# Kernel optimization log

Hardware: AMD Instinct MI355X
Metric: run time of the kernel (lower is better)

Reference implementation:

```python
import jax, jax.numpy as jnp
import numpy as np

B, N, D = 8, 2048, 768
LN_EPS = 1e-5


def setup_inputs() -> dict:
    key = jax.random.key(0)
    ks = jax.random.split(key, 5)
    scale = 1.0 / np.sqrt(D)
    features = jax.random.normal(ks[0], (B, N, D), dtype=jnp.float32)
    mask = jax.random.randint(ks[1], (B, N), 0, 2) == 1  # True = masked (padding)
    Wq = jax.random.normal(ks[2], (D, D), dtype=jnp.float32) * scale
    Wk = jax.random.normal(ks[3], (D, D), dtype=jnp.float32) * scale
    Wv = jax.random.normal(ks[4], (D, D), dtype=jnp.float32) * scale
    ln_gamma = jnp.ones((D,), dtype=jnp.float32)
    ln_beta = jnp.zeros((D,), dtype=jnp.float32)
    return {"features": features, "mask": mask, "Wq": Wq, "Wk": Wk, "Wv": Wv,
            "ln_gamma": ln_gamma, "ln_beta": ln_beta}


def reference(features, mask, Wq, Wk, Wv, ln_gamma, ln_beta):
    # LayerNorm over last dim
    mu = jnp.mean(features, axis=-1, keepdims=True)
    var = jnp.mean(jnp.square(features - mu), axis=-1, keepdims=True)
    x = (features - mu) * jax.lax.rsqrt(var + LN_EPS) * ln_gamma + ln_beta
    # torch Linear: y = x @ W.T
    Q = jnp.einsum('bnd,ed->bne', x, Wq)
    K = jnp.einsum('bnd,ed->bne', x, Wk)
    V = jnp.einsum('bnd,ed->bne', x, Wv)
    scale = x.shape[-1] ** -0.5
    scores = jnp.einsum('bnd,bmd->bnm', Q, K) * scale  # [B,N,N]
    scores = jnp.where(mask[:, None, :], -jnp.inf, scores)
    probs = jax.nn.softmax(scores, axis=-1)
    ctx = jnp.einsum('bnm,bmd->bnd', probs, V)
    return ctx
```

## Files before the change

### kernel.cpp

```cpp
#include <hip/hip_runtime.h>
#include <hip/hip_bf16.h>
#include <cstdint>

typedef __attribute__((ext_vector_type(8))) __bf16 bf16v8;
typedef __attribute__((ext_vector_type(4))) float f32x4;
typedef __attribute__((ext_vector_type(4))) unsigned short ushort4v;
typedef __attribute__((ext_vector_type(8))) unsigned short ushort8v;

#define BB 8
#define NN 2048
#define DD 768

__device__ __forceinline__ float b2f(unsigned short u) {
  union { unsigned int i; float f; } c; c.i = ((unsigned int)u) << 16; return c.f;
}
__device__ __forceinline__ unsigned short f2b(float f) {
  union { float f; unsigned int i; } c; c.f = f;
  unsigned int u = c.i;
  return (unsigned short)((u + 0x7fffu + ((u >> 16) & 1u)) >> 16);
}

__global__ __launch_bounds__(256) void ln_kernel(const float* __restrict__ x,
                                                 const float* __restrict__ gamma,
                                                 const float* __restrict__ beta,
                                                 unsigned short* __restrict__ xb) {
  int row = blockIdx.x;
  const float* xr = x + (size_t)row * DD;
  int t = threadIdx.x;
  float a0 = xr[t], a1 = xr[t + 256], a2 = xr[t + 512];
  float s = a0 + a1 + a2;
  float q = a0 * a0 + a1 * a1 + a2 * a2;
  for (int o = 32; o > 0; o >>= 1) { s += __shfl_xor(s, o); q += __shfl_xor(q, o); }
  __shared__ float red[2][4];
  int w = t >> 6, lane = t & 63;
  if (lane == 0) { red[0][w] = s; red[1][w] = q; }
  __syncthreads();
  s = red[0][0] + red[0][1] + red[0][2] + red[0][3];
  q = red[1][0] + red[1][1] + red[1][2] + red[1][3];
  float mean = s * (1.0f / DD);
  float var = q * (1.0f / DD) - mean * mean;
  float inv = rsqrtf(var + 1e-5f);
  unsigned short* o0 = xb + (size_t)row * DD;
  o0[t]       = f2b((a0 - mean) * inv * gamma[t]       + beta[t]);
  o0[t + 256] = f2b((a1 - mean) * inv * gamma[t + 256] + beta[t + 256]);
  o0[t + 512] = f2b((a2 - mean) * inv * gamma[t + 512] + beta[t + 512]);
}

__global__ __launch_bounds__(256) void wconvert(const float* __restrict__ Wq,
                                                const float* __restrict__ Wk,
                                                const float* __restrict__ Wv,
                                                unsigned short* __restrict__ Wcat) {
  int i = blockIdx.x * 256 + threadIdx.x;
  const int dd = DD * DD;
  if (i >= 3 * dd) return;
  float v;
  if (i < dd)           v = Wq[i] * 0.03608439182435161f;
  else if (i < 2 * dd)  v = Wk[i - dd];
  else                  v = Wv[i - 2 * dd];
  Wcat[i] = f2b(v);
}

__global__ __launch_bounds__(256) void mask_scan(const int* __restrict__ mask,
                                                 int* __restrict__ kidx,
                                                 int* __restrict__ ncnt) {
  int b = blockIdx.x;
  const int* mr = mask + b * NN;
  int t = threadIdx.x;
#pragma unroll
  for (int j = 0; j < 8; ++j) kidx[b * NN + t * 8 + j] = 0;
  int v[8]; int s = 0;
#pragma unroll
  for (int j = 0; j < 8; ++j) { v[j] = (mr[t * 8 + j] == 0) ? 1 : 0; s += v[j]; }
  int lane = t & 63, w = t >> 6;
  int x = s;
  for (int o = 1; o < 64; o <<= 1) { int y = __shfl_up(x, o); if (lane >= o) x += y; }
  __shared__ int wsum[4];
  if (lane == 63) wsum[w] = x;
  __syncthreads();
  int base = 0;
#pragma unroll
  for (int i = 0; i < 4; ++i) if (i < w) base += wsum[i];
  int run = base + x - s;
#pragma unroll
  for (int j = 0; j < 8; ++j) { if (v[j]) kidx[b * NN + run] = t * 8 + j; run += v[j]; }
  if (t == 255) ncnt[b] = base + x;
}

__global__ __launch_bounds__(256) void xc_gather(const unsigned short* __restrict__ Xb,
                                                 const int* __restrict__ kidx,
                                                 const int* __restrict__ ncnt,
                                                 unsigned short* __restrict__ Xc) {
  const int b = blockIdx.y;
  const int nc = ncnt[b];
  const int r256 = (nc + 255) & ~255;
  const int row0 = blockIdx.x * 32;
  if (row0 >= r256) return;
  int off = 0;
#pragma unroll
  for (int i = 0; i < 8; ++i) if (i < b) off += (ncnt[i] + 255) & ~255;
  const int t = threadIdx.x;
  for (int r = 0; r < 32; ++r) {
    const int rl = row0 + r;
    unsigned short* dst = Xc + (size_t)(off + rl) * DD;
    if (t < 96) {
      if (rl < nc) {
        const unsigned short* src = Xb + ((size_t)b * NN + kidx[b * NN + rl]) * DD;
        *(ushort8v*)&dst[t * 8] = *(const ushort8v*)&src[t * 8];
      } else {
        *(ushort8v*)&dst[t * 8] = ushort8v{0, 0, 0, 0, 0, 0, 0, 0};
      }
    }
  }
}

__device__ __forceinline__ void gload_lds16(const void* g, void* l) {
  __builtin_amdgcn_global_load_lds(
      (const __attribute__((address_space(1))) void*)g,
      (__attribute__((address_space(3))) void*)(unsigned)(uintptr_t)l,
      16, 0, 0);
}

#define RDA(i0, ks, B)                                                                   \
  _Pragma("unroll")                                                                      \
  for (int i_ = 0; i_ < 4; ++i_)                                                         \
    aq[i_] = *(const bf16v8*)&smem[(B) + (ks) * 8192 + arow0 + ((i0) + i_) * 512 + kg8];
#define RDB(ks, B)                                                                       \
  _Pragma("unroll")                                                                      \
  for (int j_ = 0; j_ < NJ; ++j_)                                                        \
    bq[j_] = *(const bf16v8*)&smem[(B) + 16384 + (ks) * 8192 + brow0 + j_ * 512 + kg8];
#define MFQ(i0)                                                                          \
  _Pragma("unroll")                                                                      \
  for (int i_ = 0; i_ < 4; ++i_) {                                                       \
    _Pragma("unroll")                                                                    \
    for (int j_ = 0; j_ < NJ; ++j_)                                                      \
      acc[(i0) + i_][j_] = __builtin_amdgcn_mfma_f32_16x16x32_bf16(                      \
          aq[i_], bq[j_], acc[(i0) + i_][j_], 0, 0, 0);                                  \
  }
#define BARF asm volatile("s_barrier" ::: "memory")
#define VMC6 asm volatile("s_waitcnt vmcnt(6)" ::: "memory")
#define VMC0 asm volatile("s_waitcnt vmcnt(0)" ::: "memory")
#define P1   __builtin_amdgcn_s_setprio(1)
#define P0   __builtin_amdgcn_s_setprio(0)

#define TILEK(KT, CURB, NXTB)                                                            \
  do {                                                                                   \
    RDA(0, 0, CURB); RDB(0, CURB);                                                       \
    if ((KT) + 1 < NT) stgA((KT) + 1, 1, (NXTB));                                        \
    BARF; P1; MFQ(0); P0; BARF;                                                          \
    RDA(4, 0, CURB);                                                                     \
    if ((KT) + 1 < NT) stgB((KT) + 1, 1, (NXTB));                                        \
    BARF; P1; MFQ(4); P0;                                                                \
    VMC6; BARF;                                                                          \
    RDA(0, 1, CURB); RDB(1, CURB);                                                       \
    if ((KT) + 2 < NT) stgA((KT) + 2, 0, (CURB));                                        \
    BARF; P1; MFQ(0); P0; BARF;                                                          \
    RDA(4, 1, CURB);                                                                     \
    if ((KT) + 2 < NT) stgB((KT) + 2, 0, (CURB));                                        \
    BARF; P1; MFQ(4); P0;                                                                \
    if ((KT) < NT - 2) { VMC6; } else { VMC0; }                                          \
    BARF;                                                                                \
  } while (0)

template <int MODE, int NJ>
__global__ __launch_bounds__(512, 2) void gemm256(
    const unsigned short* __restrict__ A, const unsigned short* __restrict__ Bm,
    unsigned short* __restrict__ Cq, float* __restrict__ Cf,
    int K, int lda, int ldb,
    long aStride, long bStride, long cStride,
    const int* __restrict__ ncnt) {
  extern __shared__ unsigned short smem[];
  const int BN = NJ * 64;

  const int t = threadIdx.x;
  int bx = blockIdx.x, by = blockIdx.y, bz = blockIdx.z;
  {
    const int gx = gridDim.x, gy = gridDim.y;
    const int nwg = gx * gy * (int)gridDim.z;
    int id = bx + gx * (by + gy * bz);
    int sw = (id & 7) * (nwg >> 3) + (id >> 3);
    bx = sw % gx; int r2 = sw / gx;
    by = r2 % gy; bz = r2 / gy;
  }
  const int n0 = bx * BN, m0 = by * 256;
  const int NT = (MODE == 2) ? (((ncnt[bz] + 127) >> 7) << 1) : (K >> 6);

  const unsigned short* Ab = A + (size_t)bz * aStride;
  const unsigned short* Bb = Bm + (size_t)bz * bStride;

  const int lane = t & 63;
  const int w = t >> 6;
  const int wm = w >> 2, wn = w & 3;
  const int frow = lane & 15;
  const int kg8 = (lane >> 4) * 8;
  const int arow0 = (wm * 128 + frow) * 32;
  const int brow0 = (wn * (NJ * 16) + frow) * 32;

  const int srow = t >> 2;
  const int scol8 = (t & 3) * 8;
  const unsigned short* Asrc = Ab + (size_t)(m0 + srow) * lda + scol8;
  const unsigned short* Bsrc = Bb + (size_t)(n0 + srow) * ldb + scol8;
  const int sdst = w * 512;

  auto stgA = [&](int kt, int ks, int bufb) {
    const unsigned short* s = Asrc + kt * 64 + ks * 32;
    gload_lds16(s, &smem[bufb + ks * 8192 + sdst]);
    gload_lds16(s + (size_t)128 * lda, &smem[bufb + ks * 8192 + 4096 + sdst]);
  };
  auto stgB = [&](int kt, int ks, int bufb) {
    const unsigned short* s = Bsrc + kt * 64 + ks * 32;
    gload_lds16(s, &smem[bufb + 16384 + ks * 8192 + sdst]);
    gload_lds16(s + (size_t)128 * ldb, &smem[bufb + 16384 + ks * 8192 + 4096 + sdst]);
  };

  f32x4 acc[8][NJ] = {};
  bf16v8 aq[4], bq[NJ];

  stgA(0, 0, 0);     stgB(0, 0, 0);
  stgA(0, 1, 0);     stgB(0, 1, 0);
  stgA(1, 0, 32768); stgB(1, 0, 32768);
  asm volatile("s_waitcnt vmcnt(8)" ::: "memory");
  BARF;

  for (int ktp = 0; ktp < NT; ktp += 2) {
    TILEK(ktp, 0, 32768);
    TILEK(ktp + 1, 32768, 0);
  }

  const int r0 = (lane >> 4) * 4;
  const int c0 = lane & 15;
  const int mrowB = m0 + wm * 128 + r0;
  const int ncolB = n0 + wn * (NJ * 16) + c0;

  if (MODE == 3) {
#pragma unroll
    for (int i = 0; i < 8; ++i)
#pragma unroll
      for (int j = 0; j < NJ; ++j)
#pragma unroll
        for (int r = 0; r < 4; ++r)
          Cq[(size_t)(mrowB + i * 16 + r) * DD + (ncolB + j * 16)] = f2b(acc[i][j][r]);
  } else {
    float* dst = Cf + (size_t)bz * cStride;
#pragma unroll
    for (int i = 0; i < 8; ++i)
#pragma unroll
      for (int j = 0; j < NJ; ++j)
#pragma unroll
        for (int r = 0; r < 4; ++r)
          dst[(size_t)(mrowB + i * 16 + r) * DD + (ncolB + j * 16)] = acc[i][j][r];
  }
}

template <int NJ, int NTT>
__global__ __launch_bounds__(512, 2) void gemmKV(
    const unsigned short* __restrict__ Xc, const unsigned short* __restrict__ Wcat,
    unsigned short* __restrict__ Kc, unsigned short* __restrict__ Vtc,
    const int* __restrict__ ncnt) {
  extern __shared__ unsigned short smem[];
  constexpr int NT = NTT;

  int offv[9]; offv[0] = 0;
#pragma unroll
  for (int i = 0; i < 8; ++i) offv[i + 1] = offv[i] + ((ncnt[i] + 255) & ~255);
  const int GT = offv[8] >> 8;
  const int id = (int)blockIdx.x;
  if (id >= GT * 8) return;
  const int gt = id >> 3, ni = id & 7;
  int b = 0;
#pragma unroll
  for (int i = 1; i < 8; ++i) if (offv[i] <= gt * 256) b = i;
  const int off_b = offv[b];

  const int t = threadIdx.x;
  const int lane = t & 63;
  const int w = t >> 6;
  const int wm = w >> 2, wn = w & 3;
  const int frow = lane & 15;
  const int kg8 = (lane >> 4) * 8;
  const int arow0 = (wm * 128 + frow) * 32;
  const int brow0 = (wn * (NJ * 16) + frow) * 32;
  const int srow = t >> 2;
  const int scol8 = (t & 3) * 8;
  const int sdst = w * 512;

  const unsigned short* Asrc = Xc + (size_t)(gt * 256 + srow) * DD + scol8;
  const unsigned short* Bsrc = Wcat + (size_t)(768 + ni * (NJ * 64) + srow) * DD + scol8;

  auto stgA = [&](int kt, int ks, int bufb) {
    const unsigned short* s = Asrc + kt * 64 + ks * 32;
    gload_lds16(s, &smem[bufb + ks * 8192 + sdst]);
    gload_lds16(s + (size_t)128 * DD, &smem[bufb + ks * 8192 + 4096 + sdst]);
  };
  auto stgB = [&](int kt, int ks, int bufb) {
    const unsigned short* s = Bsrc + kt * 64 + ks * 32;
    gload_lds16(s, &smem[bufb + 16384 + ks * 8192 + sdst]);
    gload_lds16(s + (size_t)128 * DD, &smem[bufb + 16384 + ks * 8192 + 4096 + sdst]);
  };

  f32x4 acc[8][NJ] = {};
  bf16v8 aq[4], bq[NJ];

  stgA(0, 0, 0);     stgB(0, 0, 0);
  stgA(0, 1, 0);     stgB(0, 1, 0);
  stgA(1, 0, 32768); stgB(1, 0, 32768);
  asm volatile("s_waitcnt vmcnt(8)" ::: "memory");
  BARF;

  for (int ktp = 0; ktp < NT; ktp += 2) {
    TILEK(ktp, 0, 32768);
    TILEK(ktp + 1, 32768, 0);
  }

  const int r0 = (lane >> 4) * 4;
  const int c0 = lane & 15;
  const int rowL = wm * 128 + r0;
  const int ncolL = ni * (NJ * 64) + wn * (NJ * 16) + c0;
  const int cbase = gt * 256 - off_b + rowL;

  if (ni < 4) {
    unsigned short* dst = Kc + (size_t)b * NN * DD;
#pragma unroll
    for (int i = 0; i < 8; ++i)
#pragma unroll
      for (int j = 0; j < NJ; ++j)
#pragma unroll
        for (int r = 0; r < 4; ++r)
          dst[(size_t)(cbase + i * 16 + r) * DD + (ncolL + j * 16)] = f2b(acc[i][j][r]);
  } else {
#pragma unroll
    for (int i = 0; i < 8; ++i) {
#pragma unroll
      for (int j = 0; j < NJ; ++j) {
        const int e = ncolL + j * 16 - 768;
        ushort4v pk;
#pragma unroll
        for (int r = 0; r < 4; ++r) pk[r] = f2b(acc[i][j][r]);
        *(ushort4v*)&Vtc[((size_t)b * DD + e) * NN + cbase + i * 16] = pk;
      }
    }
  }
}

template <int NJ, int NTT>
__global__ __launch_bounds__(512, 2) void gemm1P(
    const unsigned short* __restrict__ Qa, const unsigned short* __restrict__ Kn,
    unsigned short* __restrict__ So, const int* __restrict__ ncnt, int lda, int ldb) {
  extern __shared__ unsigned short smem[];
  constexpr int NT = NTT;

  const int t = threadIdx.x;
  const int lane = t & 63;
  const int w = t >> 6;
  const int wm = w >> 2, wn = w & 3;
  const int frow = lane & 15;
  const int kg8 = (lane >> 4) * 8;
  const int arow0 = (wm * 128 + frow) * 32;
  const int brow0 = (wn * (NJ * 16) + frow) * 32;
  const int srow = t >> 2;
  const int scol8 = (t & 3) * 8;
  const int sdst = w * 512;
  const int r0 = (lane >> 4) * 4;
  const int c0 = lane & 15;

  int nbv[8];
#pragma unroll
  for (int b_ = 0; b_ < 8; ++b_) nbv[b_] = (ncnt[b_] + 255) >> 8;

  f32x4 acc[8][NJ];
  bf16v8 aq[4], bq[NJ];

#pragma unroll 1
  for (int it = 0; it < 2; ++it) {
    int rem = (int)blockIdx.x + it * 256;
    int b = 0;
#pragma unroll 1
    for (; b < 8; ++b) { int c = nbv[b] * 8; if (rem < c) break; rem -= c; }
    if (b >= 8) break;
    const int ni = rem >> 3, mi = rem & 7;
    const int m0 = mi * 256, n0 = ni * 256;

    const unsigned short* Asrc = Qa + ((size_t)b * NN + m0 + srow) * lda + scol8;
    const unsigned short* Bsrc = Kn + ((size_t)b * NN + n0 + srow) * ldb + scol8;

    auto stgA = [&](int kt, int ks, int bufb) {
      const unsigned short* s = Asrc + kt * 64 + ks * 32;
      gload_lds16(s, &smem[bufb + ks * 8192 + sdst]);
      gload_lds16(s + (size_t)128 * lda, &smem[bufb + ks * 8192 + 4096 + sdst]);
    };
    auto stgB = [&](int kt, int ks, int bufb) {
      const unsigned short* s = Bsrc + kt * 64 + ks * 32;
      gload_lds16(s, &smem[bufb + 16384 + ks * 8192 + sdst]);
      gload_lds16(s + (size_t)128 * ldb, &smem[bufb + 16384 + ks * 8192 + 4096 + sdst]);
    };

#pragma unroll
    for (int i = 0; i < 8; ++i)
#pragma unroll
      for (int j = 0; j < NJ; ++j) acc[i][j] = f32x4{0.f, 0.f, 0.f, 0.f};

    stgA(0, 0, 0);     stgB(0, 0, 0);
    stgA(0, 1, 0);     stgB(0, 1, 0);
    stgA(1, 0, 32768); stgB(1, 0, 32768);
    asm volatile("s_waitcnt vmcnt(8)" ::: "memory");
    BARF;

    for (int ktp = 0; ktp < NT; ktp += 2) {
      TILEK(ktp, 0, 32768);
      TILEK(ktp + 1, 32768, 0);
    }

    unsigned short* dst = So + (size_t)b * NN * NN;
    const int mrowB = m0 + wm * 128 + r0;
    const int ncolB = n0 + wn * (NJ * 16) + c0;
#pragma unroll
    for (int i = 0; i < 8; ++i)
#pragma unroll
      for (int j = 0; j < NJ; ++j)
#pragma unroll
        for (int r = 0; r < 4; ++r)
          dst[(size_t)(mrowB + i * 16 + r) * NN + (ncolB + j * 16)] = f2b(acc[i][j][r]);
  }
}

__global__ __launch_bounds__(256) void softmax_c(unsigned short* __restrict__ S,
                                                 const int* __restrict__ ncnt) {
  int row = blockIdx.x;
  int bb = row >> 11;
  const int nc = ncnt[bb];
  const int p128 = (nc + 127) & ~127;
  unsigned short* sr = S + (size_t)row * NN;
  int t = threadIdx.x;
  const int cbase = t * 8;

  float v[8];
  const bool anyload = cbase < nc;
  ushort8v pk;
  if (anyload) pk = *(const ushort8v*)&sr[cbase];
  float mx = -1e30f;
#pragma unroll
  for (int j = 0; j < 8; ++j) {
    v[j] = anyload ? b2f(pk[j]) : 0.f;
    if (cbase + j < nc) mx = fmaxf(mx, v[j]);
  }
  for (int o = 32; o > 0; o >>= 1) mx = fmaxf(mx, __shfl_xor(mx, o));
  __shared__ float redm[4], reds[4];
  int w = t >> 6, lane = t & 63;
  if (lane == 0) redm[w] = mx;
  __syncthreads();
  mx = fmaxf(fmaxf(redm[0], redm[1]), fmaxf(redm[2], redm[3]));

  float e[8];
  float sum = 0.f;
#pragma unroll
  for (int j = 0; j < 8; ++j) {
    e[j] = (cbase + j < nc) ? __expf(v[j] - mx) : 0.f;
    sum += e[j];
  }
  for (int o = 32; o > 0; o >>= 1) sum += __shfl_xor(sum, o);
  if (lane == 0) reds[w] = sum;
  __syncthreads();
  sum = reds[0] + reds[1] + reds[2] + reds[3];
  float inv = 1.0f / sum;

  if (cbase < p128) {
    ushort8v op;
#pragma unroll
    for (int j = 0; j < 8; ++j) op[j] = f2b(e[j] * inv);
    *(ushort8v*)&sr[cbase] = op;
  }
}

extern "C" void kernel_launch(void* const* d_in, const int* in_sizes, int n_in,
                              void* d_out, int out_size, void* d_ws, size_t ws_size,
                              hipStream_t stream) {
  const float* features = (const float*)d_in[0];
  const int* mask       = (const int*)d_in[1];
  const float* Wq       = (const float*)d_in[2];
  const float* Wk       = (const float*)d_in[3];
  const float* Wv       = (const float*)d_in[4];
  const float* gamma    = (const float*)d_in[5];
  const float* beta     = (const float*)d_in[6];
  float* out = (float*)d_out;

  char* ws = (char*)d_ws;
  size_t off = 0;
  auto alloc = [&](size_t bytes) {
    char* p = ws + off;
    off += (bytes + 255) & ~(size_t)255;
    return p;
  };
  unsigned short* Wcat = (unsigned short*)alloc((size_t)(2304 + 64) * DD * 2);
  unsigned short* Qb   = (unsigned short*)alloc((size_t)BB * NN * DD * 2);
  unsigned short* Kc   = (unsigned short*)alloc((size_t)BB * NN * DD * 2);
  unsigned short* Vtc  = (unsigned short*)alloc(((size_t)BB * DD + 64) * NN * 2);
  int* kidx = (int*)alloc((size_t)BB * NN * 4);
  int* ncnt = (int*)alloc(64 * 4);
  char* last = alloc((size_t)BB * NN * NN * 2);
  unsigned short* Sb = (unsigned short*)last;
  unsigned short* Xb = (unsigned short*)last;
  unsigned short* Xc = (unsigned short*)(last + (size_t)34 * 1024 * 1024);

  (void)hipFuncSetAttribute(reinterpret_cast<const void*>(&gemm256<3, 3>),
                            hipFuncAttributeMaxDynamicSharedMemorySize, 131072);
  (void)hipFuncSetAttribute(reinterpret_cast<const void*>(&gemmKV<3, 12>),
                            hipFuncAttributeMaxDynamicSharedMemorySize, 131072);
  (void)hipFuncSetAttribute(reinterpret_cast<const void*>(&gemm1P<4, 12>),
                            hipFuncAttributeMaxDynamicSharedMemorySize, 131072);
  (void)hipFuncSetAttribute(reinterpret_cast<const void*>(&gemm256<2, 3>),
                            hipFuncAttributeMaxDynamicSharedMemorySize, 131072);

  ln_kernel<<<BB * NN, 256, 0, stream>>>(features, gamma, beta, Xb);
  wconvert<<<(3 * DD * DD + 255) / 256, 256, 0, stream>>>(Wq, Wk, Wv, Wcat);
  mask_scan<<<BB, 256, 0, stream>>>(mask, kidx, ncnt);
  xc_gather<<<dim3(64, BB), 256, 0, stream>>>(Xb, kidx, ncnt, Xc);

  gemm256<3, 3><<<dim3(4, 64, 1), 512, 131072, stream>>>(
      Xb, Wcat, Qb, nullptr, DD, DD, DD, 0, 0, 0, ncnt);

  gemmKV<3, 12><<<512, 512, 131072, stream>>>(Xc, Wcat, Kc, Vtc, ncnt);

  gemm1P<4, 12><<<256, 512, 131072, stream>>>(Qb, Kc, Sb, ncnt, DD, DD);

  softmax_c<<<BB * NN, 256, 0, stream>>>(Sb, ncnt);

  gemm256<2, 3><<<dim3(DD / 192, NN / 256, BB), 512, 131072, stream>>>(
      Sb, Vtc, nullptr, out, NN, NN, NN,
      (long)NN * NN, (long)DD * NN, (long)NN * DD, ncnt);
}
```

Before: 223.5 us.

## Shrink QK^T score GEMM tile to 128x256 and use all threads in gather

The Q·K^T kernel goes from 256x256 output tiles to 128x256 tiles, with a simpler per-k-step double-buffered loop, less LDS (96KB) and half the accumulator registers. Each block now handles up to 4 tiles instead of 2. The aim is better load balance and occupancy over the variable number of unmasked key columns. The cost is lower arithmetic intensity per tile and more B-matrix reloads. Separately, the K/V row gather now spreads 16 rows across all 256 threads instead of using 96 threads over 32 rows, to raise memory parallelism.

```diff
diff --git a/kernel.cpp b/kernel.cpp
--- a/kernel.cpp
+++ b/kernel.cpp
@@ -93,23 +93,19 @@
   const int b = blockIdx.y;
   const int nc = ncnt[b];
   const int r256 = (nc + 255) & ~255;
-  const int row0 = blockIdx.x * 32;
+  const int row0 = blockIdx.x * 16;
   if (row0 >= r256) return;
   int off = 0;
 #pragma unroll
   for (int i = 0; i < 8; ++i) if (i < b) off += (ncnt[i] + 255) & ~255;
-  const int t = threadIdx.x;
-  for (int r = 0; r < 32; ++r) {
-    const int rl = row0 + r;
-    unsigned short* dst = Xc + (size_t)(off + rl) * DD;
-    if (t < 96) {
-      if (rl < nc) {
-        const unsigned short* src = Xb + ((size_t)b * NN + kidx[b * NN + rl]) * DD;
-        *(ushort8v*)&dst[t * 8] = *(const ushort8v*)&src[t * 8];
-      } else {
-        *(ushort8v*)&dst[t * 8] = ushort8v{0, 0, 0, 0, 0, 0, 0, 0};
-      }
-    }
+  for (int u = threadIdx.x; u < 16 * 96; u += 256) {
+    const int r = row0 + u / 96;
+    const int ch = (u % 96) * 8;
+    if (r >= r256) continue;
+    ushort8v val = {0, 0, 0, 0, 0, 0, 0, 0};
+    if (r < nc)
+      val = *(const ushort8v*)&Xb[((size_t)b * NN + kidx[b * NN + r]) * DD + ch];
+    *(ushort8v*)&Xc[(size_t)(off + r) * DD + ch] = val;
   }
 }
 
@@ -138,6 +134,7 @@
   }
 #define BARF asm volatile("s_barrier" ::: "memory")
 #define VMC6 asm volatile("s_waitcnt vmcnt(6)" ::: "memory")
+#define VMC3 asm volatile("s_waitcnt vmcnt(3)" ::: "memory")
 #define VMC0 asm volatile("s_waitcnt vmcnt(0)" ::: "memory")
 #define P1   __builtin_amdgcn_s_setprio(1)
 #define P0   __builtin_amdgcn_s_setprio(0)
@@ -341,12 +338,11 @@
   }
 }
 
-template <int NJ, int NTT>
 __global__ __launch_bounds__(512, 2) void gemm1P(
     const unsigned short* __restrict__ Qa, const unsigned short* __restrict__ Kn,
-    unsigned short* __restrict__ So, const int* __restrict__ ncnt, int lda, int ldb) {
+    unsigned short* __restrict__ So, const int* __restrict__ ncnt) {
   extern __shared__ unsigned short smem[];
-  constexpr int NT = NTT;
+  constexpr int NT = 12;
 
   const int t = threadIdx.x;
   const int lane = t & 63;
@@ -354,8 +350,8 @@
   const int wm = w >> 2, wn = w & 3;
   const int frow = lane & 15;
   const int kg8 = (lane >> 4) * 8;
-  const int arow0 = (wm * 128 + frow) * 32;
-  const int brow0 = (wn * (NJ * 16) + frow) * 32;
+  const int arow0 = (wm * 64 + frow) * 32;
+  const int brow0 = (wn * 64 + frow) * 32;
   const int srow = t >> 2;
   const int scol8 = (t & 3) * 8;
   const int sdst = w * 512;
@@ -366,56 +362,85 @@
 #pragma unroll
   for (int b_ = 0; b_ < 8; ++b_) nbv[b_] = (ncnt[b_] + 255) >> 8;
 
-  f32x4 acc[8][NJ];
-  bf16v8 aq[4], bq[NJ];
+  f32x4 acc[4][4];
+  bf16v8 aq[4], bq[4];
 
 #pragma unroll 1
-  for (int it = 0; it < 2; ++it) {
+  for (int it = 0; it < 4; ++it) {
     int rem = (int)blockIdx.x + it * 256;
     int b = 0;
 #pragma unroll 1
-    for (; b < 8; ++b) { int c = nbv[b] * 8; if (rem < c) break; rem -= c; }
+    for (; b < 8; ++b) { int c = nbv[b] * 16; if (rem < c) break; rem -= c; }
     if (b >= 8) break;
-    const int ni = rem >> 3, mi = rem & 7;
-    const int m0 = mi * 256, n0 = ni * 256;
-
-    const unsigned short* Asrc = Qa + ((size_t)b * NN + m0 + srow) * lda + scol8;
-    const unsigned short* Bsrc = Kn + ((size_t)b * NN + n0 + srow) * ldb + scol8;
+    const int ni = rem >> 4, mi = rem & 15;
+    const int m0 = mi * 128, n0 = ni * 256;
+
+    const unsigned short* Asrc = Qa + ((size_t)b * NN + m0 + srow) * DD + scol8;
+    const unsigned short* Bsrc = Kn + ((size_t)b * NN + n0 + srow) * DD + scol8;
 
     auto stgA = [&](int kt, int ks, int bufb) {
-      const unsigned short* s = Asrc + kt * 64 + ks * 32;
-      gload_lds16(s, &smem[bufb + ks * 8192 + sdst]);
-      gload_lds16(s + (size_t)128 * lda, &smem[bufb + ks * 8192 + 4096 + sdst]);
+      gload_lds16(Asrc + kt * 64 + ks * 32, &smem[bufb + ks * 4096 + sdst]);
     };
     auto stgB = [&](int kt, int ks, int bufb) {
       const unsigned short* s = Bsrc + kt * 64 + ks * 32;
-      gload_lds16(s, &smem[bufb + 16384 + ks * 8192 + sdst]);
-      gload_lds16(s + (size_t)128 * ldb, &smem[bufb + 16384 + ks * 8192 + 4096 + sdst]);
+      gload_lds16(s, &smem[bufb + 8192 + ks * 8192 + sdst]);
+      gload_lds16(s + (size_t)128 * DD, &smem[bufb + 8192 + ks * 8192 + 4096 + sdst]);
     };
 
 #pragma unroll
-    for (int i = 0; i < 8; ++i)
-#pragma unroll
-      for (int j = 0; j < NJ; ++j) acc[i][j] = f32x4{0.f, 0.f, 0.f, 0.f};
+    for (int i = 0; i < 4; ++i)
+#pragma unroll
+      for (int j = 0; j < 4; ++j) acc[i][j] = f32x4{0.f, 0.f, 0.f, 0.f};
 
     stgA(0, 0, 0);     stgB(0, 0, 0);
     stgA(0, 1, 0);     stgB(0, 1, 0);
-    stgA(1, 0, 32768); stgB(1, 0, 32768);
-    asm volatile("s_waitcnt vmcnt(8)" ::: "memory");
+    stgA(1, 0, 24576); stgB(1, 0, 24576);
+    VMC3;
     BARF;
 
-    for (int ktp = 0; ktp < NT; ktp += 2) {
-      TILEK(ktp, 0, 32768);
-      TILEK(ktp + 1, 32768, 0);
+#pragma unroll 1
+    for (int kt = 0; kt < NT; ++kt) {
+      const int cur = (kt & 1) ? 24576 : 0;
+      const int nxt = cur ^ 24576;
+#pragma unroll
+      for (int i_ = 0; i_ < 4; ++i_)
+        aq[i_] = *(const bf16v8*)&smem[cur + arow0 + i_ * 512 + kg8];
+#pragma unroll
+      for (int j_ = 0; j_ < 4; ++j_)
+        bq[j_] = *(const bf16v8*)&smem[cur + 8192 + brow0 + j_ * 512 + kg8];
+      if (kt + 1 < NT) { stgA(kt + 1, 1, nxt); stgB(kt + 1, 1, nxt); }
+      BARF; P1;
+#pragma unroll
+      for (int i_ = 0; i_ < 4; ++i_)
+#pragma unroll
+        for (int j_ = 0; j_ < 4; ++j_)
+          acc[i_][j_] = __builtin_amdgcn_mfma_f32_16x16x32_bf16(aq[i_], bq[j_], acc[i_][j_], 0, 0, 0);
+      P0; BARF;
+#pragma unroll
+      for (int i_ = 0; i_ < 4; ++i_)
+        aq[i_] = *(const bf16v8*)&smem[cur + 4096 + arow0 + i_ * 512 + kg8];
+#pragma unroll
+      for (int j_ = 0; j_ < 4; ++j_)
+        bq[j_] = *(const bf16v8*)&smem[cur + 16384 + brow0 + j_ * 512 + kg8];
+      if (kt + 2 < NT) { stgA(kt + 2, 0, cur); stgB(kt + 2, 0, cur); }
+      BARF; P1;
+#pragma unroll
+      for (int i_ = 0; i_ < 4; ++i_)
+#pragma unroll
+        for (int j_ = 0; j_ < 4; ++j_)
+          acc[i_][j_] = __builtin_amdgcn_mfma_f32_16x16x32_bf16(aq[i_], bq[j_], acc[i_][j_], 0, 0, 0);
+      P0;
+      if (kt < NT - 2) { VMC3; } else { VMC0; }
+      BARF;
     }
 
     unsigned short* dst = So + (size_t)b * NN * NN;
-    const int mrowB = m0 + wm * 128 + r0;
-    const int ncolB = n0 + wn * (NJ * 16) + c0;
-#pragma unroll
-    for (int i = 0; i < 8; ++i)
-#pragma unroll
-      for (int j = 0; j < NJ; ++j)
+    const int mrowB = m0 + wm * 64 + r0;
+    const int ncolB = n0 + wn * 64 + c0;
+#pragma unroll
+    for (int i = 0; i < 4; ++i)
+#pragma unroll
+      for (int j = 0; j < 4; ++j)
 #pragma unroll
         for (int r = 0; r < 4; ++r)
           dst[(size_t)(mrowB + i * 16 + r) * NN + (ncolB + j * 16)] = f2b(acc[i][j][r]);
@@ -504,22 +529,22 @@
                             hipFuncAttributeMaxDynamicSharedMemorySize, 131072);
   (void)hipFuncSetAttribute(reinterpret_cast<const void*>(&gemmKV<3, 12>),
                             hipFuncAttributeMaxDynamicSharedMemorySize, 131072);
-  (void)hipFuncSetAttribute(reinterpret_cast<const void*>(&gemm1P<4, 12>),
-                            hipFuncAttributeMaxDynamicSharedMemorySize, 131072);
+  (void)hipFuncSetAttribute(reinterpret_cast<const void*>(&gemm1P),
+                            hipFuncAttributeMaxDynamicSharedMemorySize, 98304);
   (void)hipFuncSetAttribute(reinterpret_cast<const void*>(&gemm256<2, 3>),
                             hipFuncAttributeMaxDynamicSharedMemorySize, 131072);
 
   ln_kernel<<<BB * NN, 256, 0, stream>>>(features, gamma, beta, Xb);
   wconvert<<<(3 * DD * DD + 255) / 256, 256, 0, stream>>>(Wq, Wk, Wv, Wcat);
   mask_scan<<<BB, 256, 0, stream>>>(mask, kidx, ncnt);
-  xc_gather<<<dim3(64, BB), 256, 0, stream>>>(Xb, kidx, ncnt, Xc);
+  xc_gather<<<dim3(128, BB), 256, 0, stream>>>(Xb, kidx, ncnt, Xc);
 
   gemm256<3, 3><<<dim3(4, 64, 1), 512, 131072, stream>>>(
       Xb, Wcat, Qb, nullptr, DD, DD, DD, 0, 0, 0, ncnt);
 
   gemmKV<3, 12><<<512, 512, 131072, stream>>>(Xc, Wcat, Kc, Vtc, ncnt);
 
-  gemm1P<4, 12><<<256, 512, 131072, stream>>>(Qb, Kc, Sb, ncnt, DD, DD);
+  gemm1P<<<256, 512, 98304, stream>>>(Qb, Kc, Sb, ncnt);
 
   softmax_c<<<BB * NN, 256, 0, stream>>>(Sb, ncnt);
 
```

Measured after the change: 217.4 us. -2.7%, faster.
